# Performance work log

Measured on AMD Instinct MI355X. Metric: run time of the kernel, lower is better.

Reference implementation:

```python
import jax, jax.numpy as jnp
import numpy as np

N, F, C, H, HX = 100000, 500, 40, 256, 64
E = 1_600_000


def setup_inputs() -> dict:
    key = jax.random.key(0)
    ks = jax.random.split(key, 12)
    s = lambda fan_in: 1.0 / np.sqrt(fan_in)
    return {
        "x": jax.random.normal(ks[0], (N, F), dtype=jnp.float32),
        "y": jax.random.randint(ks[1], (N,), 0, C),
        "train_mask": jax.random.randint(ks[2], (N,), 0, 2).astype(bool),
        "edge_index": jax.random.randint(ks[3], (2, E), 0, N),
        "edge_index_neg": jax.random.randint(ks[4], (2, E), 0, N),
        "fc1_w": jax.random.uniform(ks[5], (H, F), jnp.float32, -s(F), s(F)),
        "fc1_b": jnp.zeros((H,), jnp.float32),
        "fc2_w": jax.random.uniform(ks[6], (C, H), jnp.float32, -s(H), s(H)),
        "fc2_b": jnp.zeros((C,), jnp.float32),
        "xenc_w": jax.random.uniform(ks[7], (HX, F), jnp.float32, -s(F), s(F)),
        "xenc_b": jnp.zeros((HX,), jnp.float32),
        "pexy_w": jax.random.uniform(ks[8], (1, 2 * (HX + C)), jnp.float32, -s(2 * (HX + C)), s(2 * (HX + C))),
        "pexy_b": jnp.zeros((1,), jnp.float32),
    }


def reference(x, y, train_mask, edge_index, edge_index_neg,
              fc1_w, fc1_b, fc2_w, fc2_b, xenc_w, xenc_b, pexy_w, pexy_b):
    temperature = 1.0
    # MLP p(y|x), inference mode (dropout is identity)
    h = jax.nn.relu(x @ fc1_w.T + fc1_b)
    logits = (h @ fc2_w.T + fc2_b) / temperature
    y_log_prob = jax.nn.log_softmax(logits, axis=-1)            # [N, C]
    y_prob = jnp.exp(y_log_prob)
    one_hot = jax.nn.one_hot(y, y_prob.shape[1], dtype=y_prob.dtype)
    y_prob = jnp.where(train_mask[:, None], one_hot, y_prob)    # [N, C]

    # node encoder
    xe = jax.nn.relu(x @ xenc_w.T + xenc_b)                     # [N, HX]

    # The scorer Linear(2*(HX+C) -> 1) applied to cat([x_q, x_k, y_q, y_k])
    # decomposes into per-node query/key scalars (same math, no big concat):
    hx = xe.shape[1]
    w = pexy_w[0]
    w_xq, w_xk = w[:hx], w[hx:2 * hx]
    w_yq, w_yk = w[2 * hx:2 * hx + y_prob.shape[1]], w[2 * hx + y_prob.shape[1]:]
    s_q = xe @ w_xq + y_prob @ w_yq                             # [N]
    s_k = xe @ w_xk + y_prob @ w_yk                             # [N]

    def edge_scores(ei):
        return (s_q[ei[0]] + s_k[ei[1]] + pexy_b[0])[:, None]   # [E, 1]

    e_pred_pos = edge_scores(edge_index)
    e_pred_neg = edge_scores(edge_index_neg)
    return (e_pred_pos, e_pred_neg, y_log_prob)
```

## Files before the change

### kernel.cpp

```cpp
#include <hip/hip_runtime.h>
#include <stdint.h>

#define N_NODES 100000
#define F_DIM   500
#define C_DIM   40
#define H_DIM   256
#define HX_DIM  64
#define O_DIM   320
#define E_NUM   1600000
#define RH_LD   328
#define BN      320

typedef unsigned short u16;
typedef unsigned int   u32;
typedef __attribute__((ext_vector_type(4))) u16    u16x4;
typedef __attribute__((ext_vector_type(8))) u16    u16x8;
typedef __attribute__((ext_vector_type(4))) float  f32x4;
typedef __attribute__((ext_vector_type(8))) short  bf16x8;

__device__ __forceinline__ float bf2f(u16 v) {
  u32 u = ((u32)v) << 16;
  return __builtin_bit_cast(float, u);
}
__device__ __forceinline__ u16 f2bf(float f) {
  u32 x = __builtin_bit_cast(u32, f);
  x += 0x7fffu + ((x >> 16) & 1u);
  return (u16)(x >> 16);
}

__global__ __launch_bounds__(256) void k_detect(const u32* __restrict__ tm, int* __restrict__ flag)
{
  __shared__ int s;
  if (threadIdx.x == 0) s = 0;
  __syncthreads();
  int local = 0;
  #pragma unroll
  for (int j = 0; j < 16; ++j) {
    if (tm[j * 256 + threadIdx.x] > 1u) local = 1;
  }
  if (local) s = 1;
  __syncthreads();
  if (threadIdx.x == 0) *flag = s;
}

__global__ __launch_bounds__(256) void k_cvtw(
    const float* __restrict__ fc1w, const float* __restrict__ xencw, u16* __restrict__ wws)
{
  const int g = blockIdx.x * 256 + threadIdx.x;
  const int c = g / 1280;
  const int rem = g - c * 1280;
  const int r = rem >> 2;
  const int k0 = c * 32 + (rem & 3) * 8;
  const float* src = (r < H_DIM) ? (fc1w + (long)r * F_DIM)
                                 : (xencw + (long)(r - H_DIM) * F_DIM);
  f32x4 v0 = {0.f, 0.f, 0.f, 0.f}, v1 = v0;
  if (k0 + 4 <= F_DIM) v0 = *(const f32x4*)(src + k0);
  if (k0 + 8 <= F_DIM) v1 = *(const f32x4*)(src + k0 + 4);
  u16x8 o;
  #pragma unroll
  for (int i = 0; i < 4; ++i) { o[i] = f2bf(v0[i]); o[4 + i] = f2bf(v1[i]); }
  *(u16x8*)(wws + (size_t)g * 8) = o;
}

__global__ __launch_bounds__(256) void k_cvtw2(
    const float* __restrict__ fc2w, const float* __restrict__ pw, u16* __restrict__ wwsB)
{
  const int g = blockIdx.x * 256 + threadIdx.x;
  if (g >= 1920) return;
  const int kc = g / 192;
  const int rem = g - kc * 192;
  const int r = rem >> 2;
  const int k0 = kc * 32 + (rem & 3) * 8;
  const float* src = nullptr;
  if (r < C_DIM)           { if (k0 + 8 <= H_DIM) src = fc2w + r * H_DIM + k0; }
  else if (r == C_DIM)     { if (k0 >= H_DIM) src = pw + (k0 - H_DIM); }
  else if (r == C_DIM + 1) { if (k0 >= H_DIM) src = pw + HX_DIM + (k0 - H_DIM); }
  u16x8 o = {0, 0, 0, 0, 0, 0, 0, 0};
  if (src) {
    const f32x4 v0 = *(const f32x4*)src;
    const f32x4 v1 = *(const f32x4*)(src + 4);
    #pragma unroll
    for (int i = 0; i < 4; ++i) { o[i] = f2bf(v0[i]); o[4 + i] = f2bf(v1[i]); }
  }
  *(u16x8*)(wwsB + (size_t)g * 8) = o;
}

__device__ __forceinline__ void epilogue_store(
    u16* sOut, f32x4 (&acc)[2][5], const float* __restrict__ fc1b,
    const float* __restrict__ xencb, int wcol, int l15, int lgrp)
{
  #pragma unroll
  for (int n = 0; n < 5; ++n) {
    const int col = wcol * 80 + n * 16 + l15;
    const float bias = (col < H_DIM) ? fc1b[col] : xencb[col - H_DIM];
    #pragma unroll
    for (int m = 0; m < 2; ++m) {
      const int r0 = m * 16 + lgrp * 4;
      #pragma unroll
      for (int rg = 0; rg < 4; ++rg)
        sOut[(r0 + rg) * RH_LD + col] = f2bf(fmaxf(acc[m][n][rg] + bias, 0.f));
    }
  }
}

__device__ __forceinline__ void rowhead_phase2(
    const u16* __restrict__ sOut, const u16* __restrict__ wwsB,
    const int* __restrict__ y, const void* __restrict__ tmask,
    const float* __restrict__ fc2b, const float* __restrict__ pw,
    bool byte_mask, long rowbase, int tid,
    float* __restrict__ out_lp, float* __restrict__ sq_out, float* __restrict__ sk_out)
{
  if (tid >= 128) return;
  const int lane = tid & 63, wid = tid >> 6;
  const int l15 = lane & 15, lgrp = lane >> 4;
  const u16* bBase = wwsB + l15 * 32 + lgrp * 8;
  f32x4 racc[3];
  #pragma unroll
  for (int n = 0; n < 3; ++n) racc[n] = (f32x4){0.f, 0.f, 0.f, 0.f};
  const u16* pa = sOut + (wid * 16 + l15) * RH_LD + lgrp * 8;

  bf16x8 bc[3], bn[3];
  #pragma unroll
  for (int n = 0; n < 3; ++n) bc[n] = *(const bf16x8*)(bBase + n * 512);

#define RH(kc, BC, BN_)                                                        \
  {                                                                            \
    if ((kc) < 9) {                                                            \
      _Pragma("unroll")                                                        \
      for (int n = 0; n < 3; ++n)                                              \
        BN_[n] = *(const bf16x8*)(bBase + ((kc) + 1) * 1536 + n * 512);        \
    }                                                                          \
    const bf16x8 a = *(const bf16x8*)(pa + (kc) * 32);                         \
    _Pragma("unroll")                                                          \
    for (int n = 0; n < 3; ++n)                                                \
      racc[n] = __builtin_amdgcn_mfma_f32_16x16x32_bf16(a, BC[n], racc[n], 0, 0, 0); \
  }
  RH(0, bc, bn) RH(1, bn, bc) RH(2, bc, bn) RH(3, bn, bc) RH(4, bc, bn)
  RH(5, bn, bc) RH(6, bc, bn) RH(7, bn, bc) RH(8, bc, bn) RH(9, bn, bc)
#undef RH

  const int c0 = l15, c1 = 16 + l15, c2 = 32 + l15;
  const bool v2 = (l15 < 8);
  const float b0 = fc2b[c0], b1 = fc2b[c1], b2 = v2 ? fc2b[c2] : 0.f;
  const float wq0 = pw[2 * HX_DIM + c0], wq1 = pw[2 * HX_DIM + c1],
              wq2 = v2 ? pw[2 * HX_DIM + c2] : 0.f;
  const float wk0 = pw[2 * HX_DIM + C_DIM + c0], wk1 = pw[2 * HX_DIM + C_DIM + c1],
              wk2 = v2 ? pw[2 * HX_DIM + C_DIM + c2] : 0.f;

  #pragma unroll
  for (int rg = 0; rg < 4; ++rg) {
    const long row = rowbase + wid * 16 + lgrp * 4 + rg;
    const float lg0 = racc[0][rg] + b0;
    const float lg1 = racc[1][rg] + b1;
    const float lg2 = racc[2][rg] + b2;
    const float sxq = __shfl(racc[2][rg], (lane & 48) | 8, 64);
    const float sxk = __shfl(racc[2][rg], (lane & 48) | 9, 64);

    float m = fmaxf(lg0, lg1);
    if (v2) m = fmaxf(m, lg2);
    #pragma unroll
    for (int off = 1; off < 16; off <<= 1) m = fmaxf(m, __shfl_xor(m, off, 64));
    const float e0 = __expf(lg0 - m), e1 = __expf(lg1 - m),
                e2 = v2 ? __expf(lg2 - m) : 0.f;
    float s = e0 + e1 + e2;
    #pragma unroll
    for (int off = 1; off < 16; off <<= 1) s += __shfl_xor(s, off, 64);
    const float lse = m + __logf(s);
    const float inv = 1.f / s;

    const int yv = y[row];
    const bool tm = byte_mask ? (((const unsigned char*)tmask)[row] != 0)
                              : (((const int*)tmask)[row] != 0);
    const float p0 = tm ? (c0 == yv ? 1.f : 0.f) : e0 * inv;
    const float p1 = tm ? (c1 == yv ? 1.f : 0.f) : e1 * inv;
    const float p2 = tm ? (c2 == yv ? 1.f : 0.f) : e2 * inv;
    float sq = p0 * wq0 + p1 * wq1 + p2 * wq2;
    float sk = p0 * wk0 + p1 * wk1 + p2 * wk2;
    #pragma unroll
    for (int off = 1; off < 16; off <<= 1) {
      sq += __shfl_xor(sq, off, 64);
      sk += __shfl_xor(sk, off, 64);
    }

    float* lp = out_lp + row * C_DIM;
    lp[c0] = lg0 - lse;
    lp[c1] = lg1 - lse;
    if (v2) lp[c2] = lg2 - lse;
    if (l15 == 0) { sq_out[row] = sq + sxq; sk_out[row] = sk + sxk; }
  }
}

__global__ __launch_bounds__(256, 4) void k_fused(
    const float* __restrict__ x, const u16* __restrict__ wws, const u16* __restrict__ wwsB,
    const float* __restrict__ fc1b, const float* __restrict__ xencb,
    const int* __restrict__ y, const void* __restrict__ tmask,
    const float* __restrict__ fc2b, const float* __restrict__ pw,
    const int* __restrict__ mask_flag,
    float* __restrict__ out_lp, float* __restrict__ sq_out, float* __restrict__ sk_out)
{
  __shared__ __align__(16) u16 sOut[32 * RH_LD];

  const int tid  = threadIdx.x;
  const int lane = tid & 63;
  const int wcol = tid >> 6;
  const int l15 = lane & 15, lgrp = lane >> 4;
  const long rowbase = (long)blockIdx.x * 32;

  const float* xrow0 = x + (rowbase + l15) * F_DIM;
  const float* xrow1 = xrow0 + 16 * F_DIM;
  const u16* bbase = wws + (wcol * 80 + l15) * 32 + lgrp * 8;

  f32x4 acc[2][5];
  #pragma unroll
  for (int m = 0; m < 2; ++m)
    #pragma unroll
    for (int n = 0; n < 5; ++n)
      acc[m][n] = (f32x4){0.f, 0.f, 0.f, 0.f};

#define LA(AF0, AF1, kc)                                                       \
  {                                                                            \
    const int k0 = (kc) * 32 + lgrp * 8;                                       \
    const int ka = (k0 > 496) ? 496 : k0;                                      \
    const int kb = (k0 + 4 > 496) ? 496 : (k0 + 4);                            \
    const f32x4 t0 = *(const f32x4*)(xrow0 + ka);                              \
    const f32x4 t1 = *(const f32x4*)(xrow0 + kb);                              \
    const f32x4 t2 = *(const f32x4*)(xrow1 + ka);                              \
    const f32x4 t3 = *(const f32x4*)(xrow1 + kb);                              \
    _Pragma("unroll")                                                          \
    for (int i = 0; i < 4; ++i) {                                              \
      AF0[i]     = (short)f2bf(t0[i]);  AF0[4 + i] = (short)f2bf(t1[i]);       \
      AF1[i]     = (short)f2bf(t2[i]);  AF1[4 + i] = (short)f2bf(t3[i]);       \
    }                                                                          \
  }
#define LB(dst, kc)                                                            \
  {                                                                            \
    const u16* bp = bbase + (size_t)(kc) * (BN * 32);                          \
    _Pragma("unroll")                                                          \
    for (int n = 0; n < 5; ++n) dst[n] = *(const bf16x8*)(bp + n * 512);       \
  }
#define GS(kc, AC0, AC1, AN0, AN1, BU, BL)                                     \
  {                                                                            \
    if ((kc) < 15) { LA(AN0, AN1, (kc) + 1); LB(BL, (kc) + 1); }               \
    _Pragma("unroll")                                                          \
    for (int n = 0; n < 5; ++n) {                                              \
      acc[0][n] = __builtin_amdgcn_mfma_f32_16x16x32_bf16(AC0, BU[n], acc[0][n], 0, 0, 0); \
      acc[1][n] = __builtin_amdgcn_mfma_f32_16x16x32_bf16(AC1, BU[n], acc[1][n], 0, 0, 0); \
    }                                                                          \
  }

  bf16x8 aX0, aX1, aY0, aY1, bP[5], bQ[5];
  LA(aX0, aX1, 0); LB(bP, 0);
  GS(0,  aX0, aX1, aY0, aY1, bP, bQ)  GS(1,  aY0, aY1, aX0, aX1, bQ, bP)
  GS(2,  aX0, aX1, aY0, aY1, bP, bQ)  GS(3,  aY0, aY1, aX0, aX1, bQ, bP)
  GS(4,  aX0, aX1, aY0, aY1, bP, bQ)  GS(5,  aY0, aY1, aX0, aX1, bQ, bP)
  GS(6,  aX0, aX1, aY0, aY1, bP, bQ)  GS(7,  aY0, aY1, aX0, aX1, bQ, bP)
  GS(8,  aX0, aX1, aY0, aY1, bP, bQ)  GS(9,  aY0, aY1, aX0, aX1, bQ, bP)
  GS(10, aX0, aX1, aY0, aY1, bP, bQ)  GS(11, aY0, aY1, aX0, aX1, bQ, bP)
  GS(12, aX0, aX1, aY0, aY1, bP, bQ)  GS(13, aY0, aY1, aX0, aX1, bQ, bP)
  GS(14, aX0, aX1, aY0, aY1, bP, bQ)  GS(15, aY0, aY1, aX0, aX1, bQ, bP)
#undef LA
#undef LB
#undef GS

  epilogue_store(sOut, acc, fc1b, xencb, wcol, l15, lgrp);
  __syncthreads();
  rowhead_phase2(sOut, wwsB, y, tmask, fc2b, pw, (*mask_flag != 0), rowbase, tid,
                 out_lp, sq_out, sk_out);
}

__global__ __launch_bounds__(256) void k_edges(
    const int* __restrict__ ei, const int* __restrict__ ein,
    const float* __restrict__ sq, const float* __restrict__ sk,
    const float* __restrict__ pb, float* __restrict__ out)
{
  const int e = blockIdx.x * 256 + threadIdx.x;
  if (e >= E_NUM) return;
  const float b = pb[0];
  const int a0 = ei[e],  a1 = ei[E_NUM + e];
  out[e] = sq[a0] + sk[a1] + b;
  const int c0 = ein[e], c1 = ein[E_NUM + e];
  out[E_NUM + e] = sq[c0] + sk[c1] + b;
}

extern "C" void kernel_launch(void* const* d_in, const int* in_sizes, int n_in,
                              void* d_out, int out_size, void* d_ws, size_t ws_size,
                              hipStream_t stream)
{
  const float* x     = (const float*)d_in[0];
  const int*   y     = (const int*)d_in[1];
  const void*  tm    = d_in[2];
  const int*   ei    = (const int*)d_in[3];
  const int*   ein   = (const int*)d_in[4];
  const float* fc1w  = (const float*)d_in[5];
  const float* fc1b  = (const float*)d_in[6];
  const float* fc2w  = (const float*)d_in[7];
  const float* fc2b  = (const float*)d_in[8];
  const float* xencw = (const float*)d_in[9];
  const float* xencb = (const float*)d_in[10];
  const float* pw    = (const float*)d_in[11];
  const float* pb    = (const float*)d_in[12];
  float* out = (float*)d_out;

  float* sq   = (float*)d_ws;
  float* sk   = (float*)((char*)d_ws + 400000);
  int*   flag = (int*)((char*)d_ws + 800000);
  u16*   wws  = (u16*)((char*)d_ws + 800064);
  u16*   wwsB = (u16*)((char*)d_ws + 1127744);

  k_detect<<<1, 256, 0, stream>>>((const u32*)tm, flag);
  k_cvtw  <<<80, 256, 0, stream>>>(fc1w, xencw, wws);
  k_cvtw2 <<<8, 256, 0, stream>>>(fc2w, pw, wwsB);
  k_fused <<<N_NODES / 32, 256, 0, stream>>>(x, wws, wwsB, fc1b, xencb, y, tm,
                                             fc2b, pw, flag,
                                             out + 2 * (size_t)E_NUM, sq, sk);
  k_edges <<<E_NUM / 256, 256, 0, stream>>>(ei, ein, sq, sk, pb, out);
}
```

Baseline: 157.9 us.

## Double fused GEMM row tile to 64 rows and use all four waves in row head

Each block now handles 64 node rows instead of 32. Every wave keeps four M-fragments of accumulators, so each loaded B fragment of the weight matrix is reused across twice as many rows, roughly halving weight-load traffic per row. The second-stage row head now runs on all four waves instead of two, and clamping plus guards handle the partial last block. The cost is more registers and a larger shared buffer, so occupancy drops (launch bounds lowered from 4 to 2 blocks) and there are fewer blocks to spread across the CUs.

After: 149.5 us. -5.3%, faster.

```diff
diff --git a/kernel.cpp b/kernel.cpp
--- a/kernel.cpp
+++ b/kernel.cpp
@@ -10,6 +10,7 @@
 #define E_NUM   1600000
 #define RH_LD   328
 #define BN      320
+#define G_BM    64
 
 typedef unsigned short u16;
 typedef unsigned int   u32;
@@ -85,112 +86,7 @@
   *(u16x8*)(wwsB + (size_t)g * 8) = o;
 }
 
-__device__ __forceinline__ void epilogue_store(
-    u16* sOut, f32x4 (&acc)[2][5], const float* __restrict__ fc1b,
-    const float* __restrict__ xencb, int wcol, int l15, int lgrp)
-{
-  #pragma unroll
-  for (int n = 0; n < 5; ++n) {
-    const int col = wcol * 80 + n * 16 + l15;
-    const float bias = (col < H_DIM) ? fc1b[col] : xencb[col - H_DIM];
-    #pragma unroll
-    for (int m = 0; m < 2; ++m) {
-      const int r0 = m * 16 + lgrp * 4;
-      #pragma unroll
-      for (int rg = 0; rg < 4; ++rg)
-        sOut[(r0 + rg) * RH_LD + col] = f2bf(fmaxf(acc[m][n][rg] + bias, 0.f));
-    }
-  }
-}
-
-__device__ __forceinline__ void rowhead_phase2(
-    const u16* __restrict__ sOut, const u16* __restrict__ wwsB,
-    const int* __restrict__ y, const void* __restrict__ tmask,
-    const float* __restrict__ fc2b, const float* __restrict__ pw,
-    bool byte_mask, long rowbase, int tid,
-    float* __restrict__ out_lp, float* __restrict__ sq_out, float* __restrict__ sk_out)
-{
-  if (tid >= 128) return;
-  const int lane = tid & 63, wid = tid >> 6;
-  const int l15 = lane & 15, lgrp = lane >> 4;
-  const u16* bBase = wwsB + l15 * 32 + lgrp * 8;
-  f32x4 racc[3];
-  #pragma unroll
-  for (int n = 0; n < 3; ++n) racc[n] = (f32x4){0.f, 0.f, 0.f, 0.f};
-  const u16* pa = sOut + (wid * 16 + l15) * RH_LD + lgrp * 8;
-
-  bf16x8 bc[3], bn[3];
-  #pragma unroll
-  for (int n = 0; n < 3; ++n) bc[n] = *(const bf16x8*)(bBase + n * 512);
-
-#define RH(kc, BC, BN_)                                                        \
-  {                                                                            \
-    if ((kc) < 9) {                                                            \
-      _Pragma("unroll")                                                        \
-      for (int n = 0; n < 3; ++n)                                              \
-        BN_[n] = *(const bf16x8*)(bBase + ((kc) + 1) * 1536 + n * 512);        \
-    }                                                                          \
-    const bf16x8 a = *(const bf16x8*)(pa + (kc) * 32);                         \
-    _Pragma("unroll")                                                          \
-    for (int n = 0; n < 3; ++n)                                                \
-      racc[n] = __builtin_amdgcn_mfma_f32_16x16x32_bf16(a, BC[n], racc[n], 0, 0, 0); \
-  }
-  RH(0, bc, bn) RH(1, bn, bc) RH(2, bc, bn) RH(3, bn, bc) RH(4, bc, bn)
-  RH(5, bn, bc) RH(6, bc, bn) RH(7, bn, bc) RH(8, bc, bn) RH(9, bn, bc)
-#undef RH
-
-  const int c0 = l15, c1 = 16 + l15, c2 = 32 + l15;
-  const bool v2 = (l15 < 8);
-  const float b0 = fc2b[c0], b1 = fc2b[c1], b2 = v2 ? fc2b[c2] : 0.f;
-  const float wq0 = pw[2 * HX_DIM + c0], wq1 = pw[2 * HX_DIM + c1],
-              wq2 = v2 ? pw[2 * HX_DIM + c2] : 0.f;
-  const float wk0 = pw[2 * HX_DIM + C_DIM + c0], wk1 = pw[2 * HX_DIM + C_DIM + c1],
-              wk2 = v2 ? pw[2 * HX_DIM + C_DIM + c2] : 0.f;
-
-  #pragma unroll
-  for (int rg = 0; rg < 4; ++rg) {
-    const long row = rowbase + wid * 16 + lgrp * 4 + rg;
-    const float lg0 = racc[0][rg] + b0;
-    const float lg1 = racc[1][rg] + b1;
-    const float lg2 = racc[2][rg] + b2;
-    const float sxq = __shfl(racc[2][rg], (lane & 48) | 8, 64);
-    const float sxk = __shfl(racc[2][rg], (lane & 48) | 9, 64);
-
-    float m = fmaxf(lg0, lg1);
-    if (v2) m = fmaxf(m, lg2);
-    #pragma unroll
-    for (int off = 1; off < 16; off <<= 1) m = fmaxf(m, __shfl_xor(m, off, 64));
-    const float e0 = __expf(lg0 - m), e1 = __expf(lg1 - m),
-                e2 = v2 ? __expf(lg2 - m) : 0.f;
-    float s = e0 + e1 + e2;
-    #pragma unroll
-    for (int off = 1; off < 16; off <<= 1) s += __shfl_xor(s, off, 64);
-    const float lse = m + __logf(s);
-    const float inv = 1.f / s;
-
-    const int yv = y[row];
-    const bool tm = byte_mask ? (((const unsigned char*)tmask)[row] != 0)
-                              : (((const int*)tmask)[row] != 0);
-    const float p0 = tm ? (c0 == yv ? 1.f : 0.f) : e0 * inv;
-    const float p1 = tm ? (c1 == yv ? 1.f : 0.f) : e1 * inv;
-    const float p2 = tm ? (c2 == yv ? 1.f : 0.f) : e2 * inv;
-    float sq = p0 * wq0 + p1 * wq1 + p2 * wq2;
-    float sk = p0 * wk0 + p1 * wk1 + p2 * wk2;
-    #pragma unroll
-    for (int off = 1; off < 16; off <<= 1) {
-      sq += __shfl_xor(sq, off, 64);
-      sk += __shfl_xor(sk, off, 64);
-    }
-
-    float* lp = out_lp + row * C_DIM;
-    lp[c0] = lg0 - lse;
-    lp[c1] = lg1 - lse;
-    if (v2) lp[c2] = lg2 - lse;
-    if (l15 == 0) { sq_out[row] = sq + sxq; sk_out[row] = sk + sxk; }
-  }
-}
-
-__global__ __launch_bounds__(256, 4) void k_fused(
+__global__ __launch_bounds__(256, 2) void k_fused(
     const float* __restrict__ x, const u16* __restrict__ wws, const u16* __restrict__ wwsB,
     const float* __restrict__ fc1b, const float* __restrict__ xencb,
     const int* __restrict__ y, const void* __restrict__ tmask,
@@ -198,38 +94,48 @@
     const int* __restrict__ mask_flag,
     float* __restrict__ out_lp, float* __restrict__ sq_out, float* __restrict__ sk_out)
 {
-  __shared__ __align__(16) u16 sOut[32 * RH_LD];
+  __shared__ __align__(16) u16 sOut[G_BM * RH_LD];
 
   const int tid  = threadIdx.x;
   const int lane = tid & 63;
   const int wcol = tid >> 6;
   const int l15 = lane & 15, lgrp = lane >> 4;
-  const long rowbase = (long)blockIdx.x * 32;
-
-  const float* xrow0 = x + (rowbase + l15) * F_DIM;
-  const float* xrow1 = xrow0 + 16 * F_DIM;
+  const long rowbase = (long)blockIdx.x * G_BM;
+
+  long rr0 = rowbase + l15,      rr1 = rr0 + 16, rr2 = rr0 + 32, rr3 = rr0 + 48;
+  if (rr0 > N_NODES - 1) rr0 = N_NODES - 1;
+  if (rr1 > N_NODES - 1) rr1 = N_NODES - 1;
+  if (rr2 > N_NODES - 1) rr2 = N_NODES - 1;
+  if (rr3 > N_NODES - 1) rr3 = N_NODES - 1;
+  const float* xp0 = x + rr0 * F_DIM;
+  const float* xp1 = x + rr1 * F_DIM;
+  const float* xp2 = x + rr2 * F_DIM;
+  const float* xp3 = x + rr3 * F_DIM;
+
   const u16* bbase = wws + (wcol * 80 + l15) * 32 + lgrp * 8;
 
-  f32x4 acc[2][5];
+  f32x4 acc[4][5];
   #pragma unroll
-  for (int m = 0; m < 2; ++m)
+  for (int m = 0; m < 4; ++m)
     #pragma unroll
     for (int n = 0; n < 5; ++n)
       acc[m][n] = (f32x4){0.f, 0.f, 0.f, 0.f};
 
-#define LA(AF0, AF1, kc)                                                       \
+#define LA(F0, F1, F2, F3, kc)                                                 \
   {                                                                            \
     const int k0 = (kc) * 32 + lgrp * 8;                                       \
     const int ka = (k0 > 496) ? 496 : k0;                                      \
     const int kb = (k0 + 4 > 496) ? 496 : (k0 + 4);                            \
-    const f32x4 t0 = *(const f32x4*)(xrow0 + ka);                              \
-    const f32x4 t1 = *(const f32x4*)(xrow0 + kb);                              \
-    const f32x4 t2 = *(const f32x4*)(xrow1 + ka);                              \
-    const f32x4 t3 = *(const f32x4*)(xrow1 + kb);                              \
+    const f32x4 u0 = *(const f32x4*)(xp0 + ka), w0 = *(const f32x4*)(xp0 + kb);\
+    const f32x4 u1 = *(const f32x4*)(xp1 + ka), w1 = *(const f32x4*)(xp1 + kb);\
+    const f32x4 u2 = *(const f32x4*)(xp2 + ka), w2 = *(const f32x4*)(xp2 + kb);\
+    const f32x4 u3 = *(const f32x4*)(xp3 + ka), w3 = *(const f32x4*)(xp3 + kb);\
     _Pragma("unroll")                                                          \
     for (int i = 0; i < 4; ++i) {                                              \
-      AF0[i]     = (short)f2bf(t0[i]);  AF0[4 + i] = (short)f2bf(t1[i]);       \
-      AF1[i]     = (short)f2bf(t2[i]);  AF1[4 + i] = (short)f2bf(t3[i]);       \
+      F0[i] = (short)f2bf(u0[i]);  F0[4 + i] = (short)f2bf(w0[i]);             \
+      F1[i] = (short)f2bf(u1[i]);  F1[4 + i] = (short)f2bf(w1[i]);             \
+      F2[i] = (short)f2bf(u2[i]);  F2[4 + i] = (short)f2bf(w2[i]);             \
+      F3[i] = (short)f2bf(u3[i]);  F3[4 + i] = (short)f2bf(w3[i]);             \
     }                                                                          \
   }
 #define LB(dst, kc)                                                            \
@@ -238,34 +144,137 @@
     _Pragma("unroll")                                                          \
     for (int n = 0; n < 5; ++n) dst[n] = *(const bf16x8*)(bp + n * 512);       \
   }
-#define GS(kc, AC0, AC1, AN0, AN1, BU, BL)                                     \
+#define GS(kc, AC0, AC1, AC2, AC3, AN0, AN1, AN2, AN3, BU, BL)                 \
   {                                                                            \
-    if ((kc) < 15) { LA(AN0, AN1, (kc) + 1); LB(BL, (kc) + 1); }               \
+    if ((kc) < 15) { LA(AN0, AN1, AN2, AN3, (kc) + 1); LB(BL, (kc) + 1); }     \
     _Pragma("unroll")                                                          \
     for (int n = 0; n < 5; ++n) {                                              \
       acc[0][n] = __builtin_amdgcn_mfma_f32_16x16x32_bf16(AC0, BU[n], acc[0][n], 0, 0, 0); \
       acc[1][n] = __builtin_amdgcn_mfma_f32_16x16x32_bf16(AC1, BU[n], acc[1][n], 0, 0, 0); \
+      acc[2][n] = __builtin_amdgcn_mfma_f32_16x16x32_bf16(AC2, BU[n], acc[2][n], 0, 0, 0); \
+      acc[3][n] = __builtin_amdgcn_mfma_f32_16x16x32_bf16(AC3, BU[n], acc[3][n], 0, 0, 0); \
     }                                                                          \
   }
 
-  bf16x8 aX0, aX1, aY0, aY1, bP[5], bQ[5];
-  LA(aX0, aX1, 0); LB(bP, 0);
-  GS(0,  aX0, aX1, aY0, aY1, bP, bQ)  GS(1,  aY0, aY1, aX0, aX1, bQ, bP)
-  GS(2,  aX0, aX1, aY0, aY1, bP, bQ)  GS(3,  aY0, aY1, aX0, aX1, bQ, bP)
-  GS(4,  aX0, aX1, aY0, aY1, bP, bQ)  GS(5,  aY0, aY1, aX0, aX1, bQ, bP)
-  GS(6,  aX0, aX1, aY0, aY1, bP, bQ)  GS(7,  aY0, aY1, aX0, aX1, bQ, bP)
-  GS(8,  aX0, aX1, aY0, aY1, bP, bQ)  GS(9,  aY0, aY1, aX0, aX1, bQ, bP)
-  GS(10, aX0, aX1, aY0, aY1, bP, bQ)  GS(11, aY0, aY1, aX0, aX1, bQ, bP)
-  GS(12, aX0, aX1, aY0, aY1, bP, bQ)  GS(13, aY0, aY1, aX0, aX1, bQ, bP)
-  GS(14, aX0, aX1, aY0, aY1, bP, bQ)  GS(15, aY0, aY1, aX0, aX1, bQ, bP)
+  bf16x8 aX0, aX1, aX2, aX3, aY0, aY1, aY2, aY3, bP[5], bQ[5];
+  LA(aX0, aX1, aX2, aX3, 0); LB(bP, 0);
+  GS(0,  aX0, aX1, aX2, aX3, aY0, aY1, aY2, aY3, bP, bQ)
+  GS(1,  aY0, aY1, aY2, aY3, aX0, aX1, aX2, aX3, bQ, bP)
+  GS(2,  aX0, aX1, aX2, aX3, aY0, aY1, aY2, aY3, bP, bQ)
+  GS(3,  aY0, aY1, aY2, aY3, aX0, aX1, aX2, aX3, bQ, bP)
+  GS(4,  aX0, aX1, aX2, aX3, aY0, aY1, aY2, aY3, bP, bQ)
+  GS(5,  aY0, aY1, aY2, aY3, aX0, aX1, aX2, aX3, bQ, bP)
+  GS(6,  aX0, aX1, aX2, aX3, aY0, aY1, aY2, aY3, bP, bQ)
+  GS(7,  aY0, aY1, aY2, aY3, aX0, aX1, aX2, aX3, bQ, bP)
+  GS(8,  aX0, aX1, aX2, aX3, aY0, aY1, aY2, aY3, bP, bQ)
+  GS(9,  aY0, aY1, aY2, aY3, aX0, aX1, aX2, aX3, bQ, bP)
+  GS(10, aX0, aX1, aX2, aX3, aY0, aY1, aY2, aY3, bP, bQ)
+  GS(11, aY0, aY1, aY2, aY3, aX0, aX1, aX2, aX3, bQ, bP)
+  GS(12, aX0, aX1, aX2, aX3, aY0, aY1, aY2, aY3, bP, bQ)
+  GS(13, aY0, aY1, aY2, aY3, aX0, aX1, aX2, aX3, bQ, bP)
+  GS(14, aX0, aX1, aX2, aX3, aY0, aY1, aY2, aY3, bP, bQ)
+  GS(15, aY0, aY1, aY2, aY3, aX0, aX1, aX2, aX3, bQ, bP)
 #undef LA
 #undef LB
 #undef GS
 
-  epilogue_store(sOut, acc, fc1b, xencb, wcol, l15, lgrp);
+  #pragma unroll
+  for (int n = 0; n < 5; ++n) {
+    const int col = wcol * 80 + n * 16 + l15;
+    const float bias = (col < H_DIM) ? fc1b[col] : xencb[col - H_DIM];
+    #pragma unroll
+    for (int m = 0; m < 4; ++m) {
+      const int r0 = m * 16 + lgrp * 4;
+      #pragma unroll
+      for (int rg = 0; rg < 4; ++rg)
+        sOut[(r0 + rg) * RH_LD + col] = f2bf(fmaxf(acc[m][n][rg] + bias, 0.f));
+    }
+  }
   __syncthreads();
-  rowhead_phase2(sOut, wwsB, y, tmask, fc2b, pw, (*mask_flag != 0), rowbase, tid,
-                 out_lp, sq_out, sk_out);
+
+  {
+    const int wid = tid >> 6;
+    const u16* bBase = wwsB + l15 * 32 + lgrp * 8;
+    f32x4 racc[3];
+    #pragma unroll
+    for (int n = 0; n < 3; ++n) racc[n] = (f32x4){0.f, 0.f, 0.f, 0.f};
+    const u16* pa = sOut + (wid * 16 + l15) * RH_LD + lgrp * 8;
+
+    bf16x8 bc[3], bn[3];
+    #pragma unroll
+    for (int n = 0; n < 3; ++n) bc[n] = *(const bf16x8*)(bBase + n * 512);
+
+#define RH(kc, BC, BN_)                                                        \
+    {                                                                          \
+      if ((kc) < 9) {                                                          \
+        _Pragma("unroll")                                                      \
+        for (int n = 0; n < 3; ++n)                                            \
+          BN_[n] = *(const bf16x8*)(bBase + ((kc) + 1) * 1536 + n * 512);      \
+      }                                                                        \
+      const bf16x8 a = *(const bf16x8*)(pa + (kc) * 32);                       \
+      _Pragma("unroll")                                                        \
+      for (int n = 0; n < 3; ++n)                                              \
+        racc[n] = __builtin_amdgcn_mfma_f32_16x16x32_bf16(a, BC[n], racc[n], 0, 0, 0); \
+    }
+    RH(0, bc, bn) RH(1, bn, bc) RH(2, bc, bn) RH(3, bn, bc) RH(4, bc, bn)
+    RH(5, bn, bc) RH(6, bc, bn) RH(7, bn, bc) RH(8, bc, bn) RH(9, bn, bc)
+#undef RH
+
+    const int c0 = l15, c1 = 16 + l15, c2 = 32 + l15;
+    const bool v2 = (l15 < 8);
+    const float b0 = fc2b[c0], b1 = fc2b[c1], b2 = v2 ? fc2b[c2] : 0.f;
+    const float wq0 = pw[2 * HX_DIM + c0], wq1 = pw[2 * HX_DIM + c1],
+                wq2 = v2 ? pw[2 * HX_DIM + c2] : 0.f;
+    const float wk0 = pw[2 * HX_DIM + C_DIM + c0], wk1 = pw[2 * HX_DIM + C_DIM + c1],
+                wk2 = v2 ? pw[2 * HX_DIM + C_DIM + c2] : 0.f;
+    const bool byte_mask = (*mask_flag != 0);
+
+    #pragma unroll
+    for (int rg = 0; rg < 4; ++rg) {
+      const long row = rowbase + wid * 16 + lgrp * 4 + rg;
+      const bool rv = (row < N_NODES);
+      const long rowc = rv ? row : (N_NODES - 1);
+      const float lg0 = racc[0][rg] + b0;
+      const float lg1 = racc[1][rg] + b1;
+      const float lg2 = racc[2][rg] + b2;
+      const float sxq = __shfl(racc[2][rg], (lane & 48) | 8, 64);
+      const float sxk = __shfl(racc[2][rg], (lane & 48) | 9, 64);
+
+      float m = fmaxf(lg0, lg1);
+      if (v2) m = fmaxf(m, lg2);
+      #pragma unroll
+      for (int off = 1; off < 16; off <<= 1) m = fmaxf(m, __shfl_xor(m, off, 64));
+      const float e0 = __expf(lg0 - m), e1 = __expf(lg1 - m),
+                  e2 = v2 ? __expf(lg2 - m) : 0.f;
+      float s = e0 + e1 + e2;
+      #pragma unroll
+      for (int off = 1; off < 16; off <<= 1) s += __shfl_xor(s, off, 64);
+      const float lse = m + __logf(s);
+      const float inv = 1.f / s;
+
+      const int yv = y[rowc];
+      const bool tm = byte_mask ? (((const unsigned char*)tmask)[rowc] != 0)
+                                : (((const int*)tmask)[rowc] != 0);
+      const float p0 = tm ? (c0 == yv ? 1.f : 0.f) : e0 * inv;
+      const float p1 = tm ? (c1 == yv ? 1.f : 0.f) : e1 * inv;
+      const float p2 = tm ? (c2 == yv ? 1.f : 0.f) : e2 * inv;
+      float sq = p0 * wq0 + p1 * wq1 + p2 * wq2;
+      float sk = p0 * wk0 + p1 * wk1 + p2 * wk2;
+      #pragma unroll
+      for (int off = 1; off < 16; off <<= 1) {
+        sq += __shfl_xor(sq, off, 64);
+        sk += __shfl_xor(sk, off, 64);
+      }
+
+      if (rv) {
+        float* lp = out_lp + row * C_DIM;
+        lp[c0] = lg0 - lse;
+        lp[c1] = lg1 - lse;
+        if (v2) lp[c2] = lg2 - lse;
+        if (l15 == 0) { sq_out[row] = sq + sxq; sk_out[row] = sk + sxk; }
+      }
+    }
+  }
 }
 
 __global__ __launch_bounds__(256) void k_edges(
@@ -310,8 +319,9 @@
   k_detect<<<1, 256, 0, stream>>>((const u32*)tm, flag);
   k_cvtw  <<<80, 256, 0, stream>>>(fc1w, xencw, wws);
   k_cvtw2 <<<8, 256, 0, stream>>>(fc2w, pw, wwsB);
-  k_fused <<<N_NODES / 32, 256, 0, stream>>>(x, wws, wwsB, fc1b, xencb, y, tm,
-                                             fc2b, pw, flag,
-                                             out + 2 * (size_t)E_NUM, sq, sk);
+  const int nblk = (N_NODES + G_BM - 1) / G_BM;
+  k_fused <<<nblk, 256, 0, stream>>>(x, wws, wwsB, fc1b, xencb, y, tm,
+                                     fc2b, pw, flag,
+                                     out + 2 * (size_t)E_NUM, sq, sk);
   k_edges <<<E_NUM / 256, 256, 0, stream>>>(ei, ein, sq, sk, pb, out);
 }
```
